# Kernel optimization log

Hardware: AMD Instinct MI355X
Metric: run time of the kernel (lower is better)

The kernel has to match this reference:

```python
import jax, jax.numpy as jnp
import numpy as np

B, S, C_IN, D, H = 16, 1024, 1280, 512, 8
HD = D // H  # head dim = 64
EPS = 1e-5


def _rope(x):
    # x: [b, h, s, d]; half-split rotation as in the torch module
    d = x.shape[-1]
    half = d // 2
    s = x.shape[2]
    inv_freq = 1.0 / (10000.0 ** (jnp.arange(0, d, 2, dtype=jnp.float32) / d))  # [half]
    ang = jnp.arange(s, dtype=jnp.float32)[:, None] * inv_freq[None, :]  # [s, half]
    sin, cos = jnp.sin(ang), jnp.cos(ang)  # broadcast over [b, h]
    x1, x2 = x[..., :half], x[..., half:]
    return jnp.concatenate([x1 * cos - x2 * sin, x1 * sin + x2 * cos], axis=-1)


def _ln(x, g, b):
    mu = jnp.mean(x, axis=-1, keepdims=True)
    var = jnp.mean((x - mu) ** 2, axis=-1, keepdims=True)
    return (x - mu) * jax.lax.rsqrt(var + EPS) * g + b


def setup_inputs() -> dict:
    key = jax.random.key(0)
    ks = jax.random.split(key, 12)
    def lin(k, fan_in, fan_out):
        lim = 1.0 / np.sqrt(fan_in)
        return jax.random.uniform(k, (fan_in, fan_out), jnp.float32, -lim, lim)
    return {
        "x": jax.random.normal(ks[0], (B, S, C_IN), jnp.float32),
        "w_in": lin(ks[1], C_IN, D), "b_in": jnp.zeros((D,), jnp.float32),
        "w_qkv": lin(ks[2], D, 3 * D), "b_qkv": jnp.zeros((3 * D,), jnp.float32),
        "w_out": lin(ks[3], D, D), "b_out": jnp.zeros((D,), jnp.float32),
        "w_ffn1": lin(ks[4], D, 4 * D), "b_ffn1": jnp.zeros((4 * D,), jnp.float32),
        "w_ffn2": lin(ks[5], 4 * D, D), "b_ffn2": jnp.zeros((D,), jnp.float32),
        "g1": jnp.ones((D,), jnp.float32), "bn1": jnp.zeros((D,), jnp.float32),
        "g2": jnp.ones((D,), jnp.float32), "bn2": jnp.zeros((D,), jnp.float32),
    }


def reference(x, w_in, b_in, w_qkv, b_qkv, w_out, b_out,
              w_ffn1, b_ffn1, w_ffn2, b_ffn2, g1, bn1, g2, bn2):
    h = x @ w_in + b_in  # [b, s, D]
    qkv = (h @ w_qkv + b_qkv).reshape(B, S, 3, H, HD)
    q, k, v = (jnp.transpose(qkv[:, :, i], (0, 2, 1, 3)) for i in range(3))  # [b, h, s, d]
    q, k = _rope(q), _rope(k)
    scores = jnp.einsum('bhqd,bhkd->bhqk', q, k) / np.sqrt(HD)
    attn = jax.nn.softmax(scores, axis=-1)
    o = jnp.einsum('bhqk,bhkd->bhqd', attn, v)
    o = jnp.transpose(o, (0, 2, 1, 3)).reshape(B, S, D)
    o = o @ w_out + b_out
    h = _ln(h + o, g1, bn1)
    ffn = jax.nn.relu(h @ w_ffn1 + b_ffn1) @ w_ffn2 + b_ffn2
    return _ln(h + ffn, g2, bn2)
```

## Files before the change

kernel.cpp:

```cpp
#include <hip/hip_runtime.h>
#include <hip/hip_bf16.h>
#include <math.h>

#define B_   16
#define S_   1024
#define CIN  1280
#define D_   512
#define H_   8
#define HD_  64
#define NROW (B_ * S_)

typedef __bf16 bf16;
typedef float  f32x2  __attribute__((ext_vector_type(2)));
typedef float  f32x4  __attribute__((ext_vector_type(4)));
typedef bf16   bf16x4 __attribute__((ext_vector_type(4)));
typedef bf16   bf16x8 __attribute__((ext_vector_type(8)));

__device__ __forceinline__ void gload_lds16(const bf16* g, bf16* l) {
    __builtin_amdgcn_global_load_lds(
        (const __attribute__((address_space(1))) void*)g,
        (__attribute__((address_space(3))) void*)l, 16, 0, 0);
}

#define SBAR()   __builtin_amdgcn_s_barrier()
#define SCHED0() __builtin_amdgcn_sched_barrier(0)
#define VMCNT8() asm volatile("s_waitcnt vmcnt(8)" ::: "memory")
#define VMCNT6() asm volatile("s_waitcnt vmcnt(6)" ::: "memory")
#define VMCNT2() asm volatile("s_waitcnt vmcnt(2)" ::: "memory")
#define VMCNT0() asm volatile("s_waitcnt vmcnt(0)" ::: "memory")
#define LGKM0()  asm volatile("s_waitcnt lgkmcnt(0)" ::: "memory")

__global__ void cvt_kernel(const float* __restrict__ in, bf16* __restrict__ out, int n4)
{
    int i = blockIdx.x * blockDim.x + threadIdx.x;
    if (i >= n4) return;
    f32x4 v = *(const f32x4*)(in + (size_t)i * 4);
    bf16x4 o;
    o[0] = (bf16)v[0]; o[1] = (bf16)v[1]; o[2] = (bf16)v[2]; o[3] = (bf16)v[3];
    *(bf16x4*)(out + (size_t)i * 4) = o;
}

__global__ __launch_bounds__(256)
void tr_cvt_kernel(const float* __restrict__ in, bf16* __restrict__ out, int R, int C)
{
    __shared__ float T[32][33];
    const int r0 = blockIdx.y << 5, c0 = blockIdx.x << 5;
    const int t  = threadIdx.x;
    {
        int lr = t >> 3, lc = (t & 7) << 2;
        f32x4 v = *(const f32x4*)(in + (size_t)(r0 + lr) * C + c0 + lc);
        T[lr][lc] = v[0]; T[lr][lc + 1] = v[1]; T[lr][lc + 2] = v[2]; T[lr][lc + 3] = v[3];
    }
    __syncthreads();
    {
        int oc = t >> 3, orr = (t & 7) << 2;
        bf16x4 o;
        o[0] = (bf16)T[orr][oc];     o[1] = (bf16)T[orr + 1][oc];
        o[2] = (bf16)T[orr + 2][oc]; o[3] = (bf16)T[orr + 3][oc];
        *(bf16x4*)(out + (size_t)(c0 + oc) * R + r0 + orr) = o;
    }
}

__global__ void cs_kernel(float* __restrict__ cs)
{
    int idx = blockIdx.x * 256 + threadIdx.x;
    int s = idx >> 5, i = idx & 31;
    float freq = exp2f(-(float)i * (13.287712379549449f / 32.f));
    float sn, c;
    sincosf((float)s * freq, &sn, &c);
    cs[(size_t)idx * 2]     = c;
    cs[(size_t)idx * 2 + 1] = sn;
}

#define ASZ (256 * 64)

template<int BN, bool RELU, bool RES, bool OUTF, bool OUTB>
__global__ __launch_bounds__(512, 2)
void gemm256_kernel(const bf16* __restrict__ A, const bf16* __restrict__ Wt,
                    const float* __restrict__ bias, const bf16* __restrict__ res,
                    float* __restrict__ outf, bf16* __restrict__ outb,
                    int M, int N, int K)
{
    constexpr int BSZ = BN * 64;
    constexpr int NJ  = BN / 64;
    constexpr int BCHV = (BN / 8) / 8;
    __shared__ bf16 lds[2 * ASZ + 2 * BSZ];

    const int tid  = threadIdx.x;
    const int lane = tid & 63;
    const int wid  = tid >> 6;

    const int mTiles = M >> 8;
    const int perX   = mTiles >> 3;
    const int lin    = blockIdx.x;
    const int idx    = lin >> 3;
    const int my     = (lin & 7) * perX + (idx & (perX - 1));
    const int nx     = idx / perX;
    const int m0     = my << 8, n0 = nx * BN;

    const int sRow = lane >> 3;
    const int sK   = ((lane & 7) ^ (lane >> 3)) << 3;

    const int r2 = wid >> 2;
    const int c4 = wid & 3;
    const int cc = lane & 15;
    const int g  = (lane >> 4) & 3;
    const int swz = (cc & 7) << 4;

    f32x4 acc[8][NJ] = {};

    auto stage = [&](int t, int b) {
        const bf16* gA = A  + (size_t)m0 * K + t * 64;
        const bf16* gB = Wt + (size_t)n0 * K + t * 64;
        bf16* lA = lds + b * ASZ;
        bf16* lB = lds + 2 * ASZ + b * BSZ;
        #pragma unroll
        for (int v = 0; v < 4; ++v) {
            const int ch = v * 8 + wid;
            gload_lds16(gA + (size_t)(ch * 8 + sRow) * K + sK, lA + ch * 512);
        }
        #pragma unroll
        for (int v = 0; v < BCHV; ++v) {
            const int ch = v * 8 + wid;
            gload_lds16(gB + (size_t)(ch * 8 + sRow) * K + sK, lB + ch * 512);
        }
    };

    const int T = K >> 6;
    stage(0, 0);
    stage(1, 1);
    if constexpr (BN == 256) VMCNT8(); else VMCNT6();
    SCHED0();
    SBAR();

    for (int t = 0; t < T; ++t) {
        const int b = t & 1;
        const char* lA = (const char*)(lds + b * ASZ);
        const char* lB = (const char*)(lds + 2 * ASZ + b * BSZ);

        #pragma unroll
        for (int ks = 0; ks < 2; ++ks) {
            bf16x8 af[8], bfr[NJ];
            #pragma unroll
            for (int i = 0; i < 8; ++i) {
                const int row = r2 * 128 + i * 16 + cc;
                af[i] = *(const bf16x8*)(lA + row * 128 + ((ks * 64 + g * 16) ^ swz));
            }
            #pragma unroll
            for (int j = 0; j < NJ; ++j) {
                const int row = c4 * (BN / 4) + j * 16 + cc;
                bfr[j] = *(const bf16x8*)(lB + row * 128 + ((ks * 64 + g * 16) ^ swz));
            }
            __builtin_amdgcn_s_setprio(1);
            #pragma unroll
            for (int i = 0; i < 8; ++i)
                #pragma unroll
                for (int j = 0; j < NJ; ++j)
                    acc[i][j] = __builtin_amdgcn_mfma_f32_16x16x32_bf16(af[i], bfr[j], acc[i][j], 0, 0, 0);
            __builtin_amdgcn_s_setprio(0);
        }
        SCHED0();
        SBAR();
        if (t + 2 < T) {
            stage(t + 2, b);
            if constexpr (BN == 256) VMCNT8(); else VMCNT6();
        } else if (t + 1 < T) {
            VMCNT0();
        }
        if (t + 1 < T) { SCHED0(); SBAR(); }
    }

    const int rq = g << 2;
    #pragma unroll
    for (int i = 0; i < 8; ++i) {
        #pragma unroll
        for (int j = 0; j < NJ; ++j) {
            const int gn = n0 + c4 * (BN / 4) + j * 16 + cc;
            const float bv = bias[gn];
            #pragma unroll
            for (int r = 0; r < 4; ++r) {
                const int gm = m0 + r2 * 128 + i * 16 + rq + r;
                float v = acc[i][j][r] + bv;
                if (RES)  v += (float)res[(size_t)gm * N + gn];
                if (RELU) v = fmaxf(v, 0.f);
                if (OUTF) outf[(size_t)gm * N + gn] = v;
                if (OUTB) outb[(size_t)gm * N + gn] = (bf16)v;
            }
        }
    }
}

#define LDA8(I0, BUF) do {                                                         \
    const char* _p = (const char*)ldsA + (BUF) * 32768;                            \
    _Pragma("unroll")                                                              \
    for (int _i = 0; _i < 4; ++_i) {                                               \
        const int _row = r2 * 128 + ((I0) + _i) * 16 + cc;                         \
        _Pragma("unroll")                                                          \
        for (int _k = 0; _k < 2; ++_k)                                             \
            aF[_i][_k] = *(const bf16x8*)(_p + _row * 128 + ((_k * 64 + g16) ^ swz)); \
    }                                                                              \
} while (0)

#define LDB8(J0, BUF) do {                                                         \
    const char* _p = (const char*)ldsB + (BUF) * 32768;                            \
    _Pragma("unroll")                                                              \
    for (int _j = 0; _j < 2; ++_j) {                                               \
        const int _row = c4 * 64 + ((J0) + _j) * 16 + cc;                          \
        _Pragma("unroll")                                                          \
        for (int _k = 0; _k < 2; ++_k)                                             \
            bF[_j][_k] = *(const bf16x8*)(_p + _row * 128 + ((_k * 64 + g16) ^ swz)); \
    }                                                                              \
} while (0)

#define MM8(I0, J0) do {                                                           \
    __builtin_amdgcn_s_setprio(1);                                                 \
    _Pragma("unroll")                                                              \
    for (int _i = 0; _i < 4; ++_i)                                                 \
        _Pragma("unroll")                                                          \
        for (int _j = 0; _j < 2; ++_j)                                             \
            _Pragma("unroll")                                                      \
            for (int _k = 0; _k < 2; ++_k)                                         \
                acc[(I0) + _i][(J0) + _j] = __builtin_amdgcn_mfma_f32_16x16x32_bf16( \
                    aF[_i][_k], bF[_j][_k], acc[(I0) + _i][(J0) + _j], 0, 0, 0);   \
    __builtin_amdgcn_s_setprio(0);                                                 \
} while (0)

template<int EPI, bool RELU>
__global__ __launch_bounds__(512, 2)
void gemm8p_kernel(const bf16* __restrict__ A, const bf16* __restrict__ Wt,
                   const float* __restrict__ bias, bf16* __restrict__ outb,
                   const float* __restrict__ cs, bf16* __restrict__ vt,
                   int M, int N, int K)
{
    __shared__ bf16 ldsA[2 * 256 * 64];
    __shared__ bf16 ldsB[2 * 256 * 64];

    const int tid  = threadIdx.x;
    const int lane = tid & 63;
    const int wid  = tid >> 6;

    const int mTiles = M >> 8;
    const int perX   = mTiles >> 3;
    const int lin    = blockIdx.x;
    const int idx    = lin >> 3;
    const int my     = (lin & 7) * perX + (idx & (perX - 1));
    const int nx     = idx / perX;
    const int m0     = my << 8, n0 = nx << 8;

    const int sRow8 = lane >> 3;
    const int sOff  = ((lane & 7) ^ sRow8) << 3;

    const int r2  = wid >> 2;
    const int c4  = wid & 3;
    const int cc  = lane & 15;
    const int g16 = ((lane >> 4) & 3) << 4;
    const int swz = (cc & 7) << 4;

    f32x4 acc[8][4] = {};
    bf16x8 aF[4][2], bF[2][2];

    const int T = K >> 6;

    auto stA = [&](int t, int half) {
        const bf16* gp = A + (size_t)m0 * K + t * 64;
        bf16* lp = ldsA + (t & 1) * 16384;
        #pragma unroll
        for (int ld = 0; ld < 2; ++ld) {
            const int rb = ld * 128 + half * 64 + wid * 8;
            gload_lds16(gp + (size_t)(rb + sRow8) * K + sOff, lp + rb * 64 + lane * 8);
        }
    };
    auto stB = [&](int t, int half) {
        const bf16* gp = Wt + (size_t)n0 * K + t * 64;
        bf16* lp = ldsB + (t & 1) * 16384;
        #pragma unroll
        for (int ld = 0; ld < 2; ++ld) {
            const int q  = ld * 2 + (wid >> 2);
            const int rb = q * 64 + half * 32 + (wid & 3) * 8;
            gload_lds16(gp + (size_t)(rb + sRow8) * K + sOff, lp + rb * 64 + lane * 8);
        }
    };

    stA(0, 0); stB(0, 1); stA(0, 1); stB(0, 0);
    stA(1, 0); stB(1, 1); stA(1, 1);
    VMCNT6();
    SCHED0();
    SBAR();
    SCHED0();

    for (int t = 0; t < T; ++t) {
        const int b = t & 1;
        LDA8(0, b); LDB8(0, b);
        if (t + 1 < T) stB(t + 1, 0);
        SBAR(); LGKM0(); SCHED0();
        MM8(0, 0);
        SCHED0(); SBAR();
        LDB8(2, b);
        if (t + 2 < T) stA(t + 2, 0);
        SBAR(); LGKM0(); SCHED0();
        MM8(0, 2);
        SCHED0(); SBAR();
        LDA8(4, b);
        if (t + 2 < T) stB(t + 2, 1);
        SBAR(); LGKM0(); SCHED0();
        MM8(4, 2);
        SCHED0(); SBAR();
        LDB8(0, b);
        if (t + 2 < T) stA(t + 2, 1);
        SBAR(); LGKM0(); SCHED0();
        MM8(4, 0);
        SCHED0();
        if (t + 2 < T) { VMCNT6(); } else { VMCNT0(); }
        SBAR();
        SCHED0();
    }

    const int rq = ((lane >> 4) & 3) << 2;
    if constexpr (EPI == 1) {
        if (nx < 4) {
            float bj[4];
            #pragma unroll
            for (int j = 0; j < 4; ++j) bj[j] = bias[n0 + c4 * 64 + j * 16 + cc];
            #pragma unroll
            for (int i = 0; i < 8; ++i) {
                #pragma unroll
                for (int r = 0; r < 4; ++r) {
                    const int gm = m0 + r2 * 128 + i * 16 + rq + r;
                    const int s  = gm & (S_ - 1);
                    #pragma unroll
                    for (int jp = 0; jp < 2; ++jp) {
                        const int d = jp * 16 + cc;
                        f32x2 csv = *(const f32x2*)(cs + ((size_t)s * 32 + d) * 2);
                        float x1 = acc[i][jp][r]     + bj[jp];
                        float x2 = acc[i][jp + 2][r] + bj[jp + 2];
                        const size_t o1 = (size_t)gm * N + n0 + c4 * 64 + d;
                        outb[o1]      = (bf16)(x1 * csv[0] - x2 * csv[1]);
                        outb[o1 + 32] = (bf16)(x1 * csv[1] + x2 * csv[0]);
                    }
                }
            }
        } else {
            const int hw = (nx - 4) * 4 + c4;
            const int bb = m0 >> 10;
            bf16* vbase = vt + (size_t)(bb * 8 + hw) * (HD_ * S_);
            const int sb0 = (m0 & (S_ - 1)) + r2 * 128 + rq;
            #pragma unroll
            for (int i = 0; i < 8; ++i) {
                #pragma unroll
                for (int j = 0; j < 4; ++j) {
                    const int d = j * 16 + cc;
                    const float bv = bias[n0 + c4 * 64 + d];
                    bf16x4 pk;
                    #pragma unroll
                    for (int r = 0; r < 4; ++r) pk[r] = (bf16)(acc[i][j][r] + bv);
                    *(bf16x4*)(vbase + (size_t)d * S_ + sb0 + i * 16) = pk;
                }
            }
        }
    } else {
        #pragma unroll
        for (int i = 0; i < 8; ++i) {
            #pragma unroll
            for (int j = 0; j < 4; ++j) {
                const int gn = n0 + c4 * 64 + j * 16 + cc;
                const float bv = bias[gn];
                #pragma unroll
                for (int r = 0; r < 4; ++r) {
                    const int gm = m0 + r2 * 128 + i * 16 + rq + r;
                    float v = acc[i][j][r] + bv;
                    if (RELU) v = fmaxf(v, 0.f);
                    outb[(size_t)gm * N + gn] = (bf16)v;
                }
            }
        }
    }
    (void)cs; (void)vt;
}

#define PST 72

__global__ __launch_bounds__(512)
void attn_kernel(const bf16* __restrict__ qkv, const bf16* __restrict__ vtg,
                 bf16* __restrict__ o)
{
    __shared__ bf16 Ks[2][4096];
    __shared__ bf16 Vs[2][4096];
    __shared__ bf16 Ps[8][16 * PST];

    const int bh  = blockIdx.x;
    const int b   = bh >> 3;
    const int h   = bh & 7;
    const int q0  = blockIdx.y << 7;
    const int tid = threadIdx.x;
    const int lane = tid & 63;
    const int w    = tid >> 6;
    const int c    = lane & 15;
    const int g    = lane >> 4;
    const int swz  = (c & 7) << 4;

    const size_t rs = 3 * D_;
    const bf16* qb = qkv + (size_t)b * S_ * rs + h * HD_;
    const bf16* kb = qb + D_;
    const bf16* vt = vtg + (size_t)bh * HD_ * S_;

    const int sRow = tid >> 3;
    const int sOff = ((tid & 7) ^ (sRow & 7)) << 3;

    bf16x8 qf[2];
    {
        const bf16* qrow = qb + (size_t)(q0 + w * 16 + c) * rs + g * 8;
        qf[0] = *(const bf16x8*)(qrow);
        qf[1] = *(const bf16x8*)(qrow + 32);
    }
    SCHED0();

    bf16x8 vones;
    {
        bf16 one = (bf16)(c == 0 ? 1.f : 0.f);
        #pragma unroll
        for (int u = 0; u < 8; ++u) vones[u] = one;
    }

    auto stage = [&](int t, int buf) {
        gload_lds16(kb + (size_t)(t * 64 + sRow) * rs + sOff, &Ks[buf][0] + (size_t)tid * 8);
        gload_lds16(vt + (size_t)sRow * S_ + t * 64 + sOff,   &Vs[buf][0] + (size_t)tid * 8);
    };

    f32x4 oa[4] = {};
    f32x4 oa5 = {};
    float m_r = -3.0e38f;
    const float CE  = 0.18033688011112042f;
    const float THR = 44.3614195558365f;

    stage(0, 0);
    stage(1, 1);
    VMCNT2();
    SCHED0();
    SBAR();

    for (int t = 0; t < 16; ++t) {
        const int buf = t & 1;
        const char* kB = (const char*)Ks[buf];
        const char* vB = (const char*)Vs[buf];

        f32x4 sa[4] = {};
        __builtin_amdgcn_s_setprio(1);
        #pragma unroll
        for (int ch = 0; ch < 2; ++ch)
            #pragma unroll
            for (int ks = 0; ks < 4; ++ks) {
                bf16x8 kf = *(const bf16x8*)(kB + (ks * 16 + c) * 128 + ((ch * 64 + g * 16) ^ swz));
                sa[ks] = __builtin_amdgcn_mfma_f32_16x16x32_bf16(kf, qf[ch], sa[ks], 0, 0, 0);
            }
        __builtin_amdgcn_s_setprio(0);

        float pmax = -3.0e38f;
        #pragma unroll
        for (int ks = 0; ks < 4; ++ks)
            pmax = fmaxf(pmax, fmaxf(fmaxf(sa[ks][0], sa[ks][1]), fmaxf(sa[ks][2], sa[ks][3])));
        pmax = fmaxf(pmax, __shfl_xor(pmax, 16, 64));
        pmax = fmaxf(pmax, __shfl_xor(pmax, 32, 64));

        if (!__all(pmax - m_r <= THR)) {
            float mnew = fmaxf(m_r, pmax);
            float sc = __builtin_amdgcn_exp2f((m_r - mnew) * CE);
            #pragma unroll
            for (int r = 0; r < 4; ++r) {
                float scr = __shfl(sc, g * 4 + r, 64);
                #pragma unroll
                for (int j = 0; j < 4; ++j) oa[j][r] *= scr;
                oa5[r] *= scr;
            }
            m_r = mnew;
        }

        const float nmCE = -m_r * CE;
        #pragma unroll
        for (int ks = 0; ks < 4; ++ks) {
            bf16x4 pb;
            #pragma unroll
            for (int r = 0; r < 4; ++r)
                pb[r] = (bf16)__builtin_amdgcn_exp2f(__builtin_fmaf(sa[ks][r], CE, nmCE));
            *(bf16x4*)&Ps[w][c * PST + ks * 16 + g * 4] = pb;
        }

        __builtin_amdgcn_s_setprio(1);
        #pragma unroll
        for (int ch = 0; ch < 2; ++ch) {
            bf16x8 pa = *(const bf16x8*)&Ps[w][c * PST + ch * 32 + g * 8];
            #pragma unroll
            for (int j = 0; j < 4; ++j) {
                bf16x8 vf = *(const bf16x8*)(vB + (j * 16 + c) * 128 + ((ch * 64 + g * 16) ^ swz));
                oa[j] = __builtin_amdgcn_mfma_f32_16x16x32_bf16(pa, vf, oa[j], 0, 0, 0);
            }
            oa5 = __builtin_amdgcn_mfma_f32_16x16x32_bf16(pa, vones, oa5, 0, 0, 0);
        }
        __builtin_amdgcn_s_setprio(0);

        SCHED0();
        SBAR();
        if (t + 2 < 16) {
            stage(t + 2, buf);
            VMCNT2();
        } else if (t + 1 < 16) {
            VMCNT0();
        }
        if (t + 1 < 16) { SCHED0(); SBAR(); }
    }

    float linv[4];
    #pragma unroll
    for (int r = 0; r < 4; ++r)
        linv[r] = 1.f / __shfl(oa5[r], lane & 48, 64);
    #pragma unroll
    for (int j = 0; j < 4; ++j)
        #pragma unroll
        for (int r = 0; r < 4; ++r) {
            int q = q0 + w * 16 + g * 4 + r;
            o[((size_t)(b * S_) + q) * D_ + h * HD_ + j * 16 + c] = (bf16)(oa[j][r] * linv[r]);
        }
}

template<bool OUTF, bool OUTB>
__global__ __launch_bounds__(256)
void ln_kernel(const float* __restrict__ in, const float* __restrict__ g,
               const float* __restrict__ be, float* __restrict__ outf,
               bf16* __restrict__ outb)
{
    const int row  = (blockIdx.x << 2) + (threadIdx.x >> 6);
    const int lane = threadIdx.x & 63;
    const float* p = in + (size_t)row * D_;
    f32x4 a  = *(const f32x4*)(p + lane * 4);
    f32x4 b2 = *(const f32x4*)(p + 256 + lane * 4);
    float s  = a[0] + a[1] + a[2] + a[3] + b2[0] + b2[1] + b2[2] + b2[3];
    float s2 = a[0]*a[0] + a[1]*a[1] + a[2]*a[2] + a[3]*a[3]
             + b2[0]*b2[0] + b2[1]*b2[1] + b2[2]*b2[2] + b2[3]*b2[3];
    #pragma unroll
    for (int off = 32; off; off >>= 1) {
        s  += __shfl_xor(s,  off, 64);
        s2 += __shfl_xor(s2, off, 64);
    }
    const float mean = s * (1.f / 512.f);
    const float var  = s2 * (1.f / 512.f) - mean * mean;
    const float rstd = rsqrtf(var + 1e-5f);

    f32x4 g0 = *(const f32x4*)(g + lane * 4);
    f32x4 g1 = *(const f32x4*)(g + 256 + lane * 4);
    f32x4 e0 = *(const f32x4*)(be + lane * 4);
    f32x4 e1 = *(const f32x4*)(be + 256 + lane * 4);
    f32x4 o0, o1;
    #pragma unroll
    for (int u = 0; u < 4; u++) {
        o0[u] = (a[u]  - mean) * rstd * g0[u] + e0[u];
        o1[u] = (b2[u] - mean) * rstd * g1[u] + e1[u];
    }
    if (OUTF) {
        float* of = outf + (size_t)row * D_;
        *(f32x4*)(of + lane * 4)       = o0;
        *(f32x4*)(of + 256 + lane * 4) = o1;
    }
    if (OUTB) {
        bf16x4 c0, c1;
        #pragma unroll
        for (int u = 0; u < 4; u++) { c0[u] = (bf16)o0[u]; c1[u] = (bf16)o1[u]; }
        bf16* ob = outb + (size_t)row * D_;
        *(bf16x4*)(ob + lane * 4)       = c0;
        *(bf16x4*)(ob + 256 + lane * 4) = c1;
    }
}

extern "C" void kernel_launch(void* const* d_in, const int* in_sizes, int n_in,
                              void* d_out, int out_size, void* d_ws, size_t ws_size,
                              hipStream_t stream)
{
    const float* x      = (const float*)d_in[0];
    const float* w_in   = (const float*)d_in[1];
    const float* b_in   = (const float*)d_in[2];
    const float* w_qkv  = (const float*)d_in[3];
    const float* b_qkv  = (const float*)d_in[4];
    const float* w_out  = (const float*)d_in[5];
    const float* b_out  = (const float*)d_in[6];
    const float* w_ffn1 = (const float*)d_in[7];
    const float* b_ffn1 = (const float*)d_in[8];
    const float* w_ffn2 = (const float*)d_in[9];
    const float* b_ffn2 = (const float*)d_in[10];
    const float* g1     = (const float*)d_in[11];
    const float* bn1    = (const float*)d_in[12];
    const float* g2     = (const float*)d_in[13];
    const float* bn2    = (const float*)d_in[14];

    char* ws = (char*)d_ws;
    constexpr size_t OFF_XB   = 0;
    constexpr size_t OFF_WIN  = OFF_XB   + 41943040ull;
    constexpr size_t OFF_WQKV = OFF_WIN  + 1310720ull;
    constexpr size_t OFF_WOUT = OFF_WQKV + 1572864ull;
    constexpr size_t OFF_WF1  = OFF_WOUT + 524288ull;
    constexpr size_t OFF_WF2  = OFF_WF1  + 2097152ull;
    constexpr size_t OFF_CS   = OFF_WF2  + 2097152ull;
    constexpr size_t OFF_HB   = OFF_CS   + 33554432ull;
    constexpr size_t OFF_QKV  = OFF_HB   + 16777216ull;
    constexpr size_t OFF_OB   = OFF_QKV  + 50331648ull;
    constexpr size_t OFF_VT   = OFF_OB   + 16777216ull;
    constexpr size_t OFF_H2B  = OFF_VT   + 33554432ull;
    constexpr size_t OFF_F1   = OFF_H2B  + 16777216ull;
    constexpr size_t OFF_T1   = OFF_XB;
    constexpr size_t OFF_T2   = OFF_QKV;

    bf16*  x_b    = (bf16*)(ws + OFF_XB);
    bf16*  win_t  = (bf16*)(ws + OFF_WIN);
    bf16*  wqkv_t = (bf16*)(ws + OFF_WQKV);
    bf16*  wout_t = (bf16*)(ws + OFF_WOUT);
    bf16*  wf1_t  = (bf16*)(ws + OFF_WF1);
    bf16*  wf2_t  = (bf16*)(ws + OFF_WF2);
    float* cs_t   = (float*)(ws + OFF_CS);
    bf16*  h_b    = (bf16*)(ws + OFF_HB);
    bf16*  qkv_b  = (bf16*)(ws + OFF_QKV);
    bf16*  o_b    = (bf16*)(ws + OFF_OB);
    bf16*  vt_g   = (bf16*)(ws + OFF_VT);
    bf16*  h2_b   = (bf16*)(ws + OFF_H2B);
    bf16*  f1_b   = (bf16*)(ws + OFF_F1);
    float* t1_f   = (float*)(ws + OFF_T1);
    float* t2_f   = (float*)(ws + OFF_T2);

    {
        int n4 = NROW * CIN / 4;
        cvt_kernel<<<(n4 + 255) / 256, 256, 0, stream>>>(x, x_b, n4);
    }
    tr_cvt_kernel<<<dim3(512/32, 1280/32), 256, 0, stream>>>(w_in,   win_t,  1280, 512);
    tr_cvt_kernel<<<dim3(1536/32, 512/32), 256, 0, stream>>>(w_qkv,  wqkv_t, 512, 1536);
    tr_cvt_kernel<<<dim3(512/32,  512/32), 256, 0, stream>>>(w_out,  wout_t, 512, 512);
    tr_cvt_kernel<<<dim3(2048/32, 512/32), 256, 0, stream>>>(w_ffn1, wf1_t,  512, 2048);
    tr_cvt_kernel<<<dim3(512/32, 2048/32), 256, 0, stream>>>(w_ffn2, wf2_t,  2048, 512);
    cs_kernel<<<128, 256, 0, stream>>>(cs_t);

    gemm256_kernel<128,false,false,false,true><<<(NROW/256) * (D_/128), 512, 0, stream>>>(
        x_b, win_t, b_in, nullptr, nullptr, h_b, NROW, D_, CIN);
    gemm8p_kernel<1,false><<<(NROW/256) * (3*D_/256), 512, 0, stream>>>(
        h_b, wqkv_t, b_qkv, qkv_b, cs_t, vt_g, NROW, 3*D_, D_);
    attn_kernel<<<dim3(B_*H_, S_/128), 512, 0, stream>>>(qkv_b, vt_g, o_b);
    gemm256_kernel<128,false,true,true,false><<<(NROW/256) * (D_/128), 512, 0, stream>>>(
        o_b, wout_t, b_out, h_b, t1_f, nullptr, NROW, D_, D_);
    ln_kernel<false,true><<<NROW/4, 256, 0, stream>>>(t1_f, g1, bn1, nullptr, h2_b);
    gemm8p_kernel<0,true><<<(NROW/256) * (4*D_/256), 512, 0, stream>>>(
        h2_b, wf1_t, b_ffn1, f1_b, nullptr, nullptr, NROW, 4*D_, D_);
    gemm256_kernel<128,false,true,true,false><<<(NROW/256) * (D_/128), 512, 0, stream>>>(
        f1_b, wf2_t, b_ffn2, h2_b, t2_f, nullptr, NROW, D_, 4*D_);
    ln_kernel<true,false><<<NROW/4, 256, 0, stream>>>(t2_f, g2, bn2, (float*)d_out, nullptr);

    (void)in_sizes; (void)n_in; (void)out_size; (void)ws_size;
}
```

Before: 300.7 us.

## Replace 256-row GEMM kernels with unified 128x128 tile GEMM for all linears

```diff
diff --git a/kernel.cpp b/kernel.cpp
--- a/kernel.cpp
+++ b/kernel.cpp
@@ -25,10 +25,8 @@
 #define SBAR()   __builtin_amdgcn_s_barrier()
 #define SCHED0() __builtin_amdgcn_sched_barrier(0)
 #define VMCNT8() asm volatile("s_waitcnt vmcnt(8)" ::: "memory")
-#define VMCNT6() asm volatile("s_waitcnt vmcnt(6)" ::: "memory")
 #define VMCNT2() asm volatile("s_waitcnt vmcnt(2)" ::: "memory")
 #define VMCNT0() asm volatile("s_waitcnt vmcnt(0)" ::: "memory")
-#define LGKM0()  asm volatile("s_waitcnt lgkmcnt(0)" ::: "memory")
 
 __global__ void cvt_kernel(const float* __restrict__ in, bf16* __restrict__ out, int n4)
 {
@@ -72,56 +70,49 @@
     cs[(size_t)idx * 2 + 1] = sn;
 }
 
-#define ASZ (256 * 64)
-
-template<int BN, bool RELU, bool RES, bool OUTF, bool OUTB>
-__global__ __launch_bounds__(512, 2)
-void gemm256_kernel(const bf16* __restrict__ A, const bf16* __restrict__ Wt,
+#define ASZ1 (128 * 64)
+
+template<int EPI, bool RELU, bool RES, bool OUTF, bool OUTB>
+__global__ __launch_bounds__(256, 2)
+void gemm128_kernel(const bf16* __restrict__ A, const bf16* __restrict__ Wt,
                     const float* __restrict__ bias, const bf16* __restrict__ res,
                     float* __restrict__ outf, bf16* __restrict__ outb,
+                    const float* __restrict__ cs, bf16* __restrict__ vt,
                     int M, int N, int K)
 {
-    constexpr int BSZ = BN * 64;
-    constexpr int NJ  = BN / 64;
-    constexpr int BCHV = (BN / 8) / 8;
-    __shared__ bf16 lds[2 * ASZ + 2 * BSZ];
+    __shared__ bf16 lds[4 * ASZ1];
 
     const int tid  = threadIdx.x;
     const int lane = tid & 63;
     const int wid  = tid >> 6;
 
-    const int mTiles = M >> 8;
-    const int perX   = mTiles >> 3;
-    const int lin    = blockIdx.x;
-    const int idx    = lin >> 3;
-    const int my     = (lin & 7) * perX + (idx & (perX - 1));
-    const int nx     = idx / perX;
-    const int m0     = my << 8, n0 = nx * BN;
+    const int perX = (M >> 7) >> 3;
+    const int lin  = blockIdx.x;
+    const int idx  = lin >> 3;
+    const int my   = (lin & 7) * perX + (idx & (perX - 1));
+    const int nx   = idx / perX;
+    const int m0   = my << 7, n0 = nx << 7;
 
     const int sRow = lane >> 3;
-    const int sK   = ((lane & 7) ^ (lane >> 3)) << 3;
-
-    const int r2 = wid >> 2;
-    const int c4 = wid & 3;
-    const int cc = lane & 15;
-    const int g  = (lane >> 4) & 3;
+    const int sK   = ((lane & 7) ^ sRow) << 3;
+
+    const int r2  = wid >> 1;
+    const int c2  = wid & 1;
+    const int cc  = lane & 15;
+    const int g   = (lane >> 4) & 3;
     const int swz = (cc & 7) << 4;
 
-    f32x4 acc[8][NJ] = {};
+    f32x4 acc[4][4] = {};
 
     auto stage = [&](int t, int b) {
         const bf16* gA = A  + (size_t)m0 * K + t * 64;
         const bf16* gB = Wt + (size_t)n0 * K + t * 64;
-        bf16* lA = lds + b * ASZ;
-        bf16* lB = lds + 2 * ASZ + b * BSZ;
+        bf16* lA = lds + b * ASZ1;
+        bf16* lB = lds + 2 * ASZ1 + b * ASZ1;
         #pragma unroll
         for (int v = 0; v < 4; ++v) {
-            const int ch = v * 8 + wid;
+            const int ch = v * 4 + wid;
             gload_lds16(gA + (size_t)(ch * 8 + sRow) * K + sK, lA + ch * 512);
-        }
-        #pragma unroll
-        for (int v = 0; v < BCHV; ++v) {
-            const int ch = v * 8 + wid;
             gload_lds16(gB + (size_t)(ch * 8 + sRow) * K + sK, lB + ch * 512);
         }
     };
@@ -129,33 +120,33 @@
     const int T = K >> 6;
     stage(0, 0);
     stage(1, 1);
-    if constexpr (BN == 256) VMCNT8(); else VMCNT6();
+    VMCNT8();
     SCHED0();
     SBAR();
 
     for (int t = 0; t < T; ++t) {
         const int b = t & 1;
-        const char* lA = (const char*)(lds + b * ASZ);
-        const char* lB = (const char*)(lds + 2 * ASZ + b * BSZ);
+        const char* lA = (const char*)(lds + b * ASZ1);
+        const char* lB = (const char*)(lds + 2 * ASZ1 + b * ASZ1);
 
         #pragma unroll
         for (int ks = 0; ks < 2; ++ks) {
-            bf16x8 af[8], bfr[NJ];
-            #pragma unroll
-            for (int i = 0; i < 8; ++i) {
-                const int row = r2 * 128 + i * 16 + cc;
+            bf16x8 af[4], bfr[4];
+            #pragma unroll
+            for (int i = 0; i < 4; ++i) {
+                const int row = r2 * 64 + i * 16 + cc;
                 af[i] = *(const bf16x8*)(lA + row * 128 + ((ks * 64 + g * 16) ^ swz));
             }
             #pragma unroll
-            for (int j = 0; j < NJ; ++j) {
-                const int row = c4 * (BN / 4) + j * 16 + cc;
+            for (int j = 0; j < 4; ++j) {
+                const int row = c2 * 64 + j * 16 + cc;
                 bfr[j] = *(const bf16x8*)(lB + row * 128 + ((ks * 64 + g * 16) ^ swz));
             }
             __builtin_amdgcn_s_setprio(1);
             #pragma unroll
-            for (int i = 0; i < 8; ++i)
+            for (int i = 0; i < 4; ++i)
                 #pragma unroll
-                for (int j = 0; j < NJ; ++j)
+                for (int j = 0; j < 4; ++j)
                     acc[i][j] = __builtin_amdgcn_mfma_f32_16x16x32_bf16(af[i], bfr[j], acc[i][j], 0, 0, 0);
             __builtin_amdgcn_s_setprio(0);
         }
@@ -163,7 +154,7 @@
         SBAR();
         if (t + 2 < T) {
             stage(t + 2, b);
-            if constexpr (BN == 256) VMCNT8(); else VMCNT6();
+            VMCNT8();
         } else if (t + 1 < T) {
             VMCNT0();
         }
@@ -171,161 +162,17 @@
     }
 
     const int rq = g << 2;
-    #pragma unroll
-    for (int i = 0; i < 8; ++i) {
-        #pragma unroll
-        for (int j = 0; j < NJ; ++j) {
-            const int gn = n0 + c4 * (BN / 4) + j * 16 + cc;
-            const float bv = bias[gn];
-            #pragma unroll
-            for (int r = 0; r < 4; ++r) {
-                const int gm = m0 + r2 * 128 + i * 16 + rq + r;
-                float v = acc[i][j][r] + bv;
-                if (RES)  v += (float)res[(size_t)gm * N + gn];
-                if (RELU) v = fmaxf(v, 0.f);
-                if (OUTF) outf[(size_t)gm * N + gn] = v;
-                if (OUTB) outb[(size_t)gm * N + gn] = (bf16)v;
-            }
-        }
-    }
-}
-
-#define LDA8(I0, BUF) do {                                                         \
-    const char* _p = (const char*)ldsA + (BUF) * 32768;                            \
-    _Pragma("unroll")                                                              \
-    for (int _i = 0; _i < 4; ++_i) {                                               \
-        const int _row = r2 * 128 + ((I0) + _i) * 16 + cc;                         \
-        _Pragma("unroll")                                                          \
-        for (int _k = 0; _k < 2; ++_k)                                             \
-            aF[_i][_k] = *(const bf16x8*)(_p + _row * 128 + ((_k * 64 + g16) ^ swz)); \
-    }                                                                              \
-} while (0)
-
-#define LDB8(J0, BUF) do {                                                         \
-    const char* _p = (const char*)ldsB + (BUF) * 32768;                            \
-    _Pragma("unroll")                                                              \
-    for (int _j = 0; _j < 2; ++_j) {                                               \
-        const int _row = c4 * 64 + ((J0) + _j) * 16 + cc;                          \
-        _Pragma("unroll")                                                          \
-        for (int _k = 0; _k < 2; ++_k)                                             \
-            bF[_j][_k] = *(const bf16x8*)(_p + _row * 128 + ((_k * 64 + g16) ^ swz)); \
-    }                                                                              \
-} while (0)
-
-#define MM8(I0, J0) do {                                                           \
-    __builtin_amdgcn_s_setprio(1);                                                 \
-    _Pragma("unroll")                                                              \
-    for (int _i = 0; _i < 4; ++_i)                                                 \
-        _Pragma("unroll")                                                          \
-        for (int _j = 0; _j < 2; ++_j)                                             \
-            _Pragma("unroll")                                                      \
-            for (int _k = 0; _k < 2; ++_k)                                         \
-                acc[(I0) + _i][(J0) + _j] = __builtin_amdgcn_mfma_f32_16x16x32_bf16( \
-                    aF[_i][_k], bF[_j][_k], acc[(I0) + _i][(J0) + _j], 0, 0, 0);   \
-    __builtin_amdgcn_s_setprio(0);                                                 \
-} while (0)
-
-template<int EPI, bool RELU>
-__global__ __launch_bounds__(512, 2)
-void gemm8p_kernel(const bf16* __restrict__ A, const bf16* __restrict__ Wt,
-                   const float* __restrict__ bias, bf16* __restrict__ outb,
-                   const float* __restrict__ cs, bf16* __restrict__ vt,
-                   int M, int N, int K)
-{
-    __shared__ bf16 ldsA[2 * 256 * 64];
-    __shared__ bf16 ldsB[2 * 256 * 64];
-
-    const int tid  = threadIdx.x;
-    const int lane = tid & 63;
-    const int wid  = tid >> 6;
-
-    const int mTiles = M >> 8;
-    const int perX   = mTiles >> 3;
-    const int lin    = blockIdx.x;
-    const int idx    = lin >> 3;
-    const int my     = (lin & 7) * perX + (idx & (perX - 1));
-    const int nx     = idx / perX;
-    const int m0     = my << 8, n0 = nx << 8;
-
-    const int sRow8 = lane >> 3;
-    const int sOff  = ((lane & 7) ^ sRow8) << 3;
-
-    const int r2  = wid >> 2;
-    const int c4  = wid & 3;
-    const int cc  = lane & 15;
-    const int g16 = ((lane >> 4) & 3) << 4;
-    const int swz = (cc & 7) << 4;
-
-    f32x4 acc[8][4] = {};
-    bf16x8 aF[4][2], bF[2][2];
-
-    const int T = K >> 6;
-
-    auto stA = [&](int t, int half) {
-        const bf16* gp = A + (size_t)m0 * K + t * 64;
-        bf16* lp = ldsA + (t & 1) * 16384;
-        #pragma unroll
-        for (int ld = 0; ld < 2; ++ld) {
-            const int rb = ld * 128 + half * 64 + wid * 8;
-            gload_lds16(gp + (size_t)(rb + sRow8) * K + sOff, lp + rb * 64 + lane * 8);
-        }
-    };
-    auto stB = [&](int t, int half) {
-        const bf16* gp = Wt + (size_t)n0 * K + t * 64;
-        bf16* lp = ldsB + (t & 1) * 16384;
-        #pragma unroll
-        for (int ld = 0; ld < 2; ++ld) {
-            const int q  = ld * 2 + (wid >> 2);
-            const int rb = q * 64 + half * 32 + (wid & 3) * 8;
-            gload_lds16(gp + (size_t)(rb + sRow8) * K + sOff, lp + rb * 64 + lane * 8);
-        }
-    };
-
-    stA(0, 0); stB(0, 1); stA(0, 1); stB(0, 0);
-    stA(1, 0); stB(1, 1); stA(1, 1);
-    VMCNT6();
-    SCHED0();
-    SBAR();
-    SCHED0();
-
-    for (int t = 0; t < T; ++t) {
-        const int b = t & 1;
-        LDA8(0, b); LDB8(0, b);
-        if (t + 1 < T) stB(t + 1, 0);
-        SBAR(); LGKM0(); SCHED0();
-        MM8(0, 0);
-        SCHED0(); SBAR();
-        LDB8(2, b);
-        if (t + 2 < T) stA(t + 2, 0);
-        SBAR(); LGKM0(); SCHED0();
-        MM8(0, 2);
-        SCHED0(); SBAR();
-        LDA8(4, b);
-        if (t + 2 < T) stB(t + 2, 1);
-        SBAR(); LGKM0(); SCHED0();
-        MM8(4, 2);
-        SCHED0(); SBAR();
-        LDB8(0, b);
-        if (t + 2 < T) stA(t + 2, 1);
-        SBAR(); LGKM0(); SCHED0();
-        MM8(4, 0);
-        SCHED0();
-        if (t + 2 < T) { VMCNT6(); } else { VMCNT0(); }
-        SBAR();
-        SCHED0();
-    }
-
-    const int rq = ((lane >> 4) & 3) << 2;
     if constexpr (EPI == 1) {
-        if (nx < 4) {
+        const int colb = c2 * 64;
+        if (nx < 8) {
             float bj[4];
             #pragma unroll
-            for (int j = 0; j < 4; ++j) bj[j] = bias[n0 + c4 * 64 + j * 16 + cc];
-            #pragma unroll
-            for (int i = 0; i < 8; ++i) {
+            for (int j = 0; j < 4; ++j) bj[j] = bias[n0 + colb + j * 16 + cc];
+            #pragma unroll
+            for (int i = 0; i < 4; ++i) {
                 #pragma unroll
                 for (int r = 0; r < 4; ++r) {
-                    const int gm = m0 + r2 * 128 + i * 16 + rq + r;
+                    const int gm = m0 + r2 * 64 + i * 16 + rq + r;
                     const int s  = gm & (S_ - 1);
                     #pragma unroll
                     for (int jp = 0; jp < 2; ++jp) {
@@ -333,23 +180,24 @@
                         f32x2 csv = *(const f32x2*)(cs + ((size_t)s * 32 + d) * 2);
                         float x1 = acc[i][jp][r]     + bj[jp];
                         float x2 = acc[i][jp + 2][r] + bj[jp + 2];
-                        const size_t o1 = (size_t)gm * N + n0 + c4 * 64 + d;
+                        const size_t o1 = (size_t)gm * N + n0 + colb + d;
                         outb[o1]      = (bf16)(x1 * csv[0] - x2 * csv[1]);
                         outb[o1 + 32] = (bf16)(x1 * csv[1] + x2 * csv[0]);
                     }
                 }
             }
         } else {
-            const int hw = (nx - 4) * 4 + c4;
+            const int col0 = n0 + colb;
+            const int hw = (col0 >> 6) & 7;
             const int bb = m0 >> 10;
             bf16* vbase = vt + (size_t)(bb * 8 + hw) * (HD_ * S_);
-            const int sb0 = (m0 & (S_ - 1)) + r2 * 128 + rq;
-            #pragma unroll
-            for (int i = 0; i < 8; ++i) {
+            const int sb0 = (m0 & (S_ - 1)) + r2 * 64 + rq;
+            #pragma unroll
+            for (int i = 0; i < 4; ++i) {
                 #pragma unroll
                 for (int j = 0; j < 4; ++j) {
                     const int d = j * 16 + cc;
-                    const float bv = bias[n0 + c4 * 64 + d];
+                    const float bv = bias[col0 + d];
                     bf16x4 pk;
                     #pragma unroll
                     for (int r = 0; r < 4; ++r) pk[r] = (bf16)(acc[i][j][r] + bv);
@@ -359,17 +207,19 @@
         }
     } else {
         #pragma unroll
-        for (int i = 0; i < 8; ++i) {
+        for (int i = 0; i < 4; ++i) {
             #pragma unroll
             for (int j = 0; j < 4; ++j) {
-                const int gn = n0 + c4 * 64 + j * 16 + cc;
+                const int gn = n0 + c2 * 64 + j * 16 + cc;
                 const float bv = bias[gn];
                 #pragma unroll
                 for (int r = 0; r < 4; ++r) {
-                    const int gm = m0 + r2 * 128 + i * 16 + rq + r;
+                    const int gm = m0 + r2 * 64 + i * 16 + rq + r;
                     float v = acc[i][j][r] + bv;
+                    if (RES)  v += (float)res[(size_t)gm * N + gn];
                     if (RELU) v = fmaxf(v, 0.f);
-                    outb[(size_t)gm * N + gn] = (bf16)v;
+                    if (OUTF) outf[(size_t)gm * N + gn] = v;
+                    if (OUTB) outb[(size_t)gm * N + gn] = (bf16)v;
                 }
             }
         }
@@ -633,18 +483,18 @@
     tr_cvt_kernel<<<dim3(512/32, 2048/32), 256, 0, stream>>>(w_ffn2, wf2_t,  2048, 512);
     cs_kernel<<<128, 256, 0, stream>>>(cs_t);
 
-    gemm256_kernel<128,false,false,false,true><<<(NROW/256) * (D_/128), 512, 0, stream>>>(
-        x_b, win_t, b_in, nullptr, nullptr, h_b, NROW, D_, CIN);
-    gemm8p_kernel<1,false><<<(NROW/256) * (3*D_/256), 512, 0, stream>>>(
-        h_b, wqkv_t, b_qkv, qkv_b, cs_t, vt_g, NROW, 3*D_, D_);
+    gemm128_kernel<0,false,false,false,true><<<(NROW/128) * (D_/128), 256, 0, stream>>>(
+        x_b, win_t, b_in, nullptr, nullptr, h_b, nullptr, nullptr, NROW, D_, CIN);
+    gemm128_kernel<1,false,false,false,true><<<(NROW/128) * (3*D_/128), 256, 0, stream>>>(
+        h_b, wqkv_t, b_qkv, nullptr, nullptr, qkv_b, cs_t, vt_g, NROW, 3*D_, D_);
     attn_kernel<<<dim3(B_*H_, S_/128), 512, 0, stream>>>(qkv_b, vt_g, o_b);
-    gemm256_kernel<128,false,true,true,false><<<(NROW/256) * (D_/128), 512, 0, stream>>>(
-        o_b, wout_t, b_out, h_b, t1_f, nullptr, NROW, D_, D_);
+    gemm128_kernel<0,false,true,true,false><<<(NROW/128) * (D_/128), 256, 0, stream>>>(
+        o_b, wout_t, b_out, h_b, t1_f, nullptr, nullptr, nullptr, NROW, D_, D_);
     ln_kernel<false,true><<<NROW/4, 256, 0, stream>>>(t1_f, g1, bn1, nullptr, h2_b);
-    gemm8p_kernel<0,true><<<(NROW/256) * (4*D_/256), 512, 0, stream>>>(
-        h2_b, wf1_t, b_ffn1, f1_b, nullptr, nullptr, NROW, 4*D_, D_);
-    gemm256_kernel<128,false,true,true,false><<<(NROW/256) * (D_/128), 512, 0, stream>>>(
-        f1_b, wf2_t, b_ffn2, h2_b, t2_f, nullptr, NROW, D_, 4*D_);
+    gemm128_kernel<0,true,false,false,true><<<(NROW/128) * (4*D_/128), 256, 0, stream>>>(
+        h2_b, wf1_t, b_ffn1, nullptr, nullptr, f1_b, nullptr, nullptr, NROW, 4*D_, D_);
+    gemm128_kernel<0,false,true,true,false><<<(NROW/128) * (D_/128), 256, 0, stream>>>(
+        f1_b, wf2_t, b_ffn2, h2_b, t2_f, nullptr, nullptr, nullptr, NROW, D_, 4*D_);
     ln_kernel<true,false><<<NROW/4, 256, 0, stream>>>(t2_f, g2, bn2, (float*)d_out, nullptr);
 
     (void)in_sizes; (void)n_in; (void)out_size; (void)ws_size;
```

After: 275.7 us. 8.3% less time.
